# Performance work log

Measured on AMD Instinct MI355X. Metric: run time of the kernel, lower is better.

## Reference

```python
import jax, jax.numpy as jnp
import numpy as np

T = 32
TAU = 2.0
ALPHA = 2.0
V_TH = 1.0
V_RESET = 0.0
PHI = 0.05
MAX_ACTION = 1.0
STATE_DIM, ACTION_DIM = 376, 17
H1, H2 = 400, 300
BATCH = 8192


@jax.custom_vjp
def spike_fn(x):
    # Heaviside with ATan surrogate gradient (spikingjelly surrogate.ATan)
    return (x >= 0.0).astype(x.dtype)

def _spike_fwd(x):
    return spike_fn(x), x

def _spike_bwd(x, g):
    return (g * (ALPHA / 2.0) / (1.0 + (jnp.pi / 2.0 * ALPHA * x) ** 2),)

spike_fn.defvjp(_spike_fwd, _spike_bwd)


def setup_inputs() -> dict:
    key = jax.random.key(0)
    ks = jax.random.split(key, 8)
    d_in = STATE_DIM + ACTION_DIM
    s = lambda k, shape, fan: jax.random.uniform(k, shape, jnp.float32, -1.0, 1.0) / np.sqrt(fan)
    return {
        "state": jax.random.normal(ks[0], (BATCH, STATE_DIM), jnp.float32),
        "action": jax.random.normal(ks[1], (BATCH, ACTION_DIM), jnp.float32),
        "W1": s(ks[2], (d_in, H1), d_in), "b1": s(ks[3], (H1,), d_in),
        "W2": s(ks[4], (H1, H2), H1),   "b2": s(ks[5], (H2,), H1),
        "W3": s(ks[6], (H2, ACTION_DIM), H2), "b3": s(ks[7], (ACTION_DIM,), H2),
    }


def reference(state, action, W1, b1, W2, b2, W3, b3):
    # input repeated over T -> layer-1 pre-activation current is step-invariant
    inp = jnp.concatenate([state, action], axis=1)          # [B, state+action]
    x1 = inp @ W1 + b1                                      # [B, H1]
    B = state.shape[0]

    def step(carry, _):
        v1, v2, v3 = carry
        # LIF layer 1: charge v += (x - (v - v_reset))/tau, fire, hard reset
        v1 = v1 + (x1 - (v1 - V_RESET)) / TAU
        s1 = spike_fn(v1 - V_TH)
        v1 = s1 * V_RESET + (1.0 - s1) * v1
        # LIF layer 2
        x2 = s1 @ W2 + b2
        v2 = v2 + (x2 - (v2 - V_RESET)) / TAU
        s2 = spike_fn(v2 - V_TH)
        v2 = s2 * V_RESET + (1.0 - s2) * v2
        # non-spiking LIF layer 3: charge only, output membrane potential
        x3 = s2 @ W3 + b3
        v3 = v3 + (x3 - (v3 - V_RESET)) / TAU
        return (v1, v2, v3), v3

    init = (jnp.full((B, H1), V_RESET, x1.dtype),
            jnp.full((B, H2), V_RESET, x1.dtype),
            jnp.full((B, ACTION_DIM), V_RESET, x1.dtype))
    _, v3_seq = jax.lax.scan(step, init, None, length=T)    # [T, B, action_dim]
    a = v3_seq.max(axis=0)
    a = PHI * MAX_ACTION * jnp.tanh(a)
    return jnp.clip(a + action, -MAX_ACTION, MAX_ACTION)
```

## Files before the change

kernel.cpp:

```cpp
#include <hip/hip_runtime.h>
#include <math.h>

#define SDIM 376
#define ADIM 17
#define DIN  393
#define H1   400
#define H2   300
#define TSTEPS 32
#define KP 416

typedef __bf16 bf16x8 __attribute__((ext_vector_type(8)));
typedef float  f32x4  __attribute__((ext_vector_type(4)));

__global__ __launch_bounds__(256) void prep_fused(
    const float* __restrict__ state, const float* __restrict__ action,
    const float* __restrict__ W1,
    __bf16* __restrict__ inpb, __bf16* __restrict__ W1T,
    int B, int npack) {
    const int bid = blockIdx.x, tid = threadIdx.x;
    if (bid < npack) {
        int idx = bid * 256 + tid;
        int r = idx / 52, c = idx - r * 52;
        if (r >= B) return;
        int g0 = c * 8;
        float v[8];
        if (g0 + 7 < SDIM) {
            float4 a = *(const float4*)&state[r * SDIM + g0];
            float4 b = *(const float4*)&state[r * SDIM + g0 + 4];
            v[0]=a.x; v[1]=a.y; v[2]=a.z; v[3]=a.w; v[4]=b.x; v[5]=b.y; v[6]=b.z; v[7]=b.w;
        } else {
            #pragma unroll
            for (int e = 0; e < 8; ++e) {
                int k = g0 + e;
                v[e] = (k < SDIM) ? state[r * SDIM + k]
                     : (k < DIN)  ? action[r * ADIM + k - SDIM] : 0.f;
            }
        }
        bf16x8 o;
        #pragma unroll
        for (int e = 0; e < 8; ++e) o[e] = (__bf16)v[e];
        *(bf16x8*)&inpb[r * KP + g0] = o;
    } else {
        int idx = (bid - npack) * 256 + tid;
        if (idx >= H1 * KP) return;
        int n = idx / KP, k = idx - n * KP;
        W1T[idx] = (__bf16)((k < DIN) ? W1[k * H1 + n] : 0.f);
    }
}

__global__ __launch_bounds__(256) void gemm_mask(
    const __bf16* __restrict__ inpb, const __bf16* __restrict__ W1T,
    const float* __restrict__ b1, unsigned short* __restrict__ maskbuf) {
    const int tid = threadIdx.x, wave = tid >> 6, lane = tid & 63;
    const int quad = lane >> 4, l16 = lane & 15;
    const int bm0 = blockIdx.x * 64 + wave * 16;
    const int bn0 = blockIdx.y * 80;

    f32x4 acc[5];
    #pragma unroll
    for (int n = 0; n < 5; ++n) acc[n] = (f32x4){0.f, 0.f, 0.f, 0.f};

    const __bf16* ap = inpb + (size_t)(bm0 + l16) * KP + quad * 8;
    const __bf16* bp = W1T + (size_t)(bn0 + l16) * KP + quad * 8;

    #pragma unroll
    for (int k0 = 0; k0 < KP; k0 += 32) {
        bf16x8 af = *(const bf16x8*)(ap + k0);
        #pragma unroll
        for (int n = 0; n < 5; ++n) {
            bf16x8 bfrag = *(const bf16x8*)(bp + n * 16 * KP + k0);
            acc[n] = __builtin_amdgcn_mfma_f32_16x16x32_bf16(af, bfrag, acc[n], 0, 0, 0);
        }
    }

    float b1v[5];
    #pragma unroll
    for (int n = 0; n < 5; ++n) b1v[n] = b1[bn0 + n * 16 + l16];
    const int cbase = bn0 >> 4;
    #pragma unroll
    for (int n = 0; n < 5; ++n)
        #pragma unroll
        for (int reg = 0; reg < 4; ++reg) {
            unsigned long long bal = __ballot(acc[n][reg] + b1v[n] >= 0.99f);
            if (l16 == 0)
                maskbuf[(size_t)(bm0 + quad * 4 + reg) * 32 + cbase + n] =
                    (unsigned short)(bal >> (quad * 16));
        }
}

__global__ __launch_bounds__(256) void snn_actor(
    const unsigned long long* __restrict__ mask64,
    const float* __restrict__ state, const float* __restrict__ action,
    const float* __restrict__ W1, const float* __restrict__ b1,
    const float* __restrict__ W2, const float* __restrict__ b2,
    const float* __restrict__ W3, const float* __restrict__ b3,
    float* __restrict__ out) {
    const int lane = threadIdx.x & 63;
    const int row  = blockIdx.x * 4 + (threadIdx.x >> 6);

    unsigned long long mw = 0;
    if (lane < 7) {
        mw = mask64[row * 8 + lane];
        if (lane == 6) mw &= 0xFFFFULL;
    }

    const float act = (lane < ADIM) ? action[row * ADIM + lane] : 0.f;
    const float b3v = (lane < ADIM) ? b3[lane] : 0.f;

    float gv;
    {
        float v3 = 0.f, vm = -3.0e38f;
        #pragma unroll
        for (int t = 0; t < TSTEPS; ++t) { v3 += (b3v - v3) * 0.5f; vm = fmaxf(vm, v3); }
        gv = 0.05f * tanhf(vm);
    }

    float bound[5];
    #pragma unroll
    for (int c = 0; c < 5; ++c) { int j = lane + 64 * c; bound[c] = (j < H2) ? b2[j] : 0.f; }
    #pragma unroll 1
    for (int w = 0; w < 7; ++w) {
        unsigned long long m = __shfl(mw, w);
        while (m) {
            int b = __builtin_ctzll(m); m &= m - 1;
            const float* wr = W2 + (w * 64 + b) * H2;
            #pragma unroll
            for (int c = 0; c < 5; ++c) {
                int j = lane + 64 * c;
                if (j < H2) bound[c] += fmaxf(wr[j], 0.f);
            }
        }
    }
    bool ok = true;
    #pragma unroll
    for (int c = 0; c < 5; ++c) ok = ok && (bound[c] < 0.999f);
    if (__all(ok)) {
        if (lane < ADIM) out[row * ADIM + lane] = fminf(fmaxf(gv + act, -1.f), 1.f);
        return;
    }

    float x1v[7];
    #pragma unroll
    for (int s = 0; s < 7; ++s) { int col = lane + 64 * s; x1v[s] = (col < H1) ? b1[col] : 0.f; }
    for (int k = 0; k < DIN; ++k) {
        float ik = (k < SDIM) ? state[row * SDIM + k] : action[row * ADIM + k - SDIM];
        #pragma unroll
        for (int s = 0; s < 7; ++s) {
            int col = lane + 64 * s;
            if (col < H1) x1v[s] += ik * W1[k * H1 + col];
        }
    }
    float b2v[5];
    #pragma unroll
    for (int c = 0; c < 5; ++c) { int j = lane + 64 * c; b2v[c] = (j < H2) ? b2[j] : 0.f; }
    float v1[7], v2[5], v3 = 0.f, vmax = -3.0e38f;
    #pragma unroll
    for (int s = 0; s < 7; ++s) v1[s] = 0.f;
    #pragma unroll
    for (int c = 0; c < 5; ++c) v2[c] = 0.f;
    for (int t = 0; t < TSTEPS; ++t) {
        float x2[5];
        #pragma unroll
        for (int c = 0; c < 5; ++c) x2[c] = b2v[c];
        #pragma unroll
        for (int s = 0; s < 7; ++s) {
            float v = v1[s] + (x1v[s] - v1[s]) * 0.5f;
            bool sp = v >= 1.0f;
            v1[s] = sp ? 0.f : v;
            unsigned long long m = __ballot(sp);
            while (m) {
                int j = __builtin_ctzll(m); m &= m - 1;
                const float* wr = W2 + (s * 64 + j) * H2;
                #pragma unroll
                for (int c = 0; c < 5; ++c) {
                    int col = lane + 64 * c;
                    if (col < H2) x2[c] += wr[col];
                }
            }
        }
        float x3 = b3v;
        #pragma unroll
        for (int c = 0; c < 5; ++c) {
            float v = v2[c] + (x2[c] - v2[c]) * 0.5f;
            int col = lane + 64 * c;
            bool sp = (col < H2) && (v >= 1.0f);
            v2[c] = sp ? 0.f : v;
            unsigned long long m = __ballot(sp);
            while (m) {
                int j = __builtin_ctzll(m); m &= m - 1;
                if (lane < ADIM) x3 += W3[(c * 64 + j) * ADIM + lane];
            }
        }
        v3 += (x3 - v3) * 0.5f;
        vmax = fmaxf(vmax, v3);
    }
    if (lane < ADIM)
        out[row * ADIM + lane] = fminf(fmaxf(0.05f * tanhf(vmax) + act, -1.f), 1.f);
}

extern "C" void kernel_launch(void* const* d_in, const int* in_sizes, int n_in,
                              void* d_out, int out_size, void* d_ws, size_t ws_size,
                              hipStream_t stream) {
    const float* state  = (const float*)d_in[0];
    const float* action = (const float*)d_in[1];
    const float* W1     = (const float*)d_in[2];
    const float* b1     = (const float*)d_in[3];
    const float* W2     = (const float*)d_in[4];
    const float* b2     = (const float*)d_in[5];
    const float* W3     = (const float*)d_in[6];
    const float* b3     = (const float*)d_in[7];
    float* out = (float*)d_out;

    const int B = in_sizes[0] / SDIM;

    char* p = (char*)d_ws;
    __bf16* inpb = (__bf16*)p;                 p += (size_t)B * KP * 2;
    __bf16* W1T  = (__bf16*)p;                 p += (size_t)H1 * KP * 2;
    unsigned short* maskbuf = (unsigned short*)p;
    unsigned long long* mask64 = (unsigned long long*)p;

    const int npack = (B * 52 + 255) / 256;
    const int nw1t  = (H1 * KP + 255) / 256;
    prep_fused<<<npack + nw1t, 256, 0, stream>>>(state, action, W1, inpb, W1T, B, npack);
    gemm_mask<<<dim3(B / 64, 5), 256, 0, stream>>>(inpb, W1T, b1, maskbuf);
    snn_actor<<<B / 4, 256, 0, stream>>>(mask64, state, action,
                                         W1, b1, W2, b2, W3, b3, out);
}
```

Before: 109.5 us.

## Fuse bf16 packing and W1 transpose into the mask GEMM kernel

Drops the separate prep kernel that converted state/action and W1 to padded bf16 buffers in workspace. The GEMM kernel now reads fp32 state/action directly, converting to bf16 in registers, and each block stages its 80-column slice of W1 into LDS in MFMA fragment order. This removes a kernel launch and the round trip of the intermediate buffers through global memory. In exchange, every block re-reads and converts the full W1 slice (B/64 times redundantly), and the first loop iteration reads from LDS slots written by a different thread.

```diff
diff --git a/kernel.cpp b/kernel.cpp
--- a/kernel.cpp
+++ b/kernel.cpp
@@ -7,83 +7,79 @@
 #define H1   400
 #define H2   300
 #define TSTEPS 32
-#define KP 416
+#define NKT 13
 
 typedef __bf16 bf16x8 __attribute__((ext_vector_type(8)));
 typedef float  f32x4  __attribute__((ext_vector_type(4)));
 
-__global__ __launch_bounds__(256) void prep_fused(
+__global__ __launch_bounds__(256) void gemm_mask_fused(
     const float* __restrict__ state, const float* __restrict__ action,
-    const float* __restrict__ W1,
-    __bf16* __restrict__ inpb, __bf16* __restrict__ W1T,
-    int B, int npack) {
-    const int bid = blockIdx.x, tid = threadIdx.x;
-    if (bid < npack) {
-        int idx = bid * 256 + tid;
-        int r = idx / 52, c = idx - r * 52;
-        if (r >= B) return;
-        int g0 = c * 8;
-        float v[8];
-        if (g0 + 7 < SDIM) {
-            float4 a = *(const float4*)&state[r * SDIM + g0];
-            float4 b = *(const float4*)&state[r * SDIM + g0 + 4];
-            v[0]=a.x; v[1]=a.y; v[2]=a.z; v[3]=a.w; v[4]=b.x; v[5]=b.y; v[6]=b.z; v[7]=b.w;
+    const float* __restrict__ W1, const float* __restrict__ b1,
+    unsigned short* __restrict__ maskbuf) {
+    __shared__ __bf16 Bf[5 * NKT * 64 * 8];
+
+    const int tid = threadIdx.x, wave = tid >> 6, lane = tid & 63;
+    const int quad = lane >> 4, l16 = lane & 15;
+    const int bm0 = blockIdx.x * 64;
+    const int bn0 = blockIdx.y * 80;
+
+    {
+        int k = tid / 80, c = tid - (tid / 80) * 80;
+        #pragma unroll 1
+        for (int i = tid; i < 416 * 80; i += 256) {
+            float v = (k < DIN) ? W1[k * H1 + bn0 + c] : 0.f;
+            int ntile = c >> 4, kt = k >> 5, q = (k >> 3) & 3, e = k & 7;
+            Bf[(((ntile * NKT + kt) * 64) + (q << 4) + (c & 15)) * 8 + e] = (__bf16)v;
+            c += 16; k += 3;
+            if (c >= 80) { c -= 80; k += 1; }
+        }
+    }
+    __syncthreads();
+
+    const int arow = bm0 + wave * 16 + l16;
+    const float* __restrict__ srow = state + (size_t)arow * SDIM;
+    const float* __restrict__ arow_p = action + (size_t)arow * ADIM;
+
+    f32x4 acc[5];
+    #pragma unroll
+    for (int n = 0; n < 5; ++n) acc[n] = (f32x4){0.f, 0.f, 0.f, 0.f};
+
+    #pragma unroll
+    for (int kt = 0; kt < NKT; ++kt) {
+        bf16x8 af;
+        const int k0 = kt * 32 + quad * 8;
+        if (kt <= 10) {
+            float4 x = *(const float4*)(srow + k0);
+            float4 y = *(const float4*)(srow + k0 + 4);
+            af[0]=(__bf16)x.x; af[1]=(__bf16)x.y; af[2]=(__bf16)x.z; af[3]=(__bf16)x.w;
+            af[4]=(__bf16)y.x; af[5]=(__bf16)y.y; af[6]=(__bf16)y.z; af[7]=(__bf16)y.w;
         } else {
             #pragma unroll
             for (int e = 0; e < 8; ++e) {
-                int k = g0 + e;
-                v[e] = (k < SDIM) ? state[r * SDIM + k]
-                     : (k < DIN)  ? action[r * ADIM + k - SDIM] : 0.f;
-            }
-        }
-        bf16x8 o;
-        #pragma unroll
-        for (int e = 0; e < 8; ++e) o[e] = (__bf16)v[e];
-        *(bf16x8*)&inpb[r * KP + g0] = o;
-    } else {
-        int idx = (bid - npack) * 256 + tid;
-        if (idx >= H1 * KP) return;
-        int n = idx / KP, k = idx - n * KP;
-        W1T[idx] = (__bf16)((k < DIN) ? W1[k * H1 + n] : 0.f);
-    }
-}
-
-__global__ __launch_bounds__(256) void gemm_mask(
-    const __bf16* __restrict__ inpb, const __bf16* __restrict__ W1T,
-    const float* __restrict__ b1, unsigned short* __restrict__ maskbuf) {
-    const int tid = threadIdx.x, wave = tid >> 6, lane = tid & 63;
-    const int quad = lane >> 4, l16 = lane & 15;
-    const int bm0 = blockIdx.x * 64 + wave * 16;
-    const int bn0 = blockIdx.y * 80;
-
-    f32x4 acc[5];
-    #pragma unroll
-    for (int n = 0; n < 5; ++n) acc[n] = (f32x4){0.f, 0.f, 0.f, 0.f};
-
-    const __bf16* ap = inpb + (size_t)(bm0 + l16) * KP + quad * 8;
-    const __bf16* bp = W1T + (size_t)(bn0 + l16) * KP + quad * 8;
-
-    #pragma unroll
-    for (int k0 = 0; k0 < KP; k0 += 32) {
-        bf16x8 af = *(const bf16x8*)(ap + k0);
+                int k = k0 + e;
+                float v = (k < SDIM) ? srow[k] : (k < DIN) ? arow_p[k - SDIM] : 0.f;
+                af[e] = (__bf16)v;
+            }
+        }
         #pragma unroll
         for (int n = 0; n < 5; ++n) {
-            bf16x8 bfrag = *(const bf16x8*)(bp + n * 16 * KP + k0);
-            acc[n] = __builtin_amdgcn_mfma_f32_16x16x32_bf16(af, bfrag, acc[n], 0, 0, 0);
+            bf16x8 bfr = *(const bf16x8*)&Bf[(((n * NKT + kt) * 64) + lane) * 8];
+            acc[n] = __builtin_amdgcn_mfma_f32_16x16x32_bf16(af, bfr, acc[n], 0, 0, 0);
         }
     }
 
     float b1v[5];
     #pragma unroll
     for (int n = 0; n < 5; ++n) b1v[n] = b1[bn0 + n * 16 + l16];
-    const int cbase = bn0 >> 4;
+    const int cbase = blockIdx.y * 5;
+    const int mbase = bm0 + wave * 16;
     #pragma unroll
     for (int n = 0; n < 5; ++n)
         #pragma unroll
         for (int reg = 0; reg < 4; ++reg) {
             unsigned long long bal = __ballot(acc[n][reg] + b1v[n] >= 0.99f);
             if (l16 == 0)
-                maskbuf[(size_t)(bm0 + quad * 4 + reg) * 32 + cbase + n] =
+                maskbuf[(size_t)(mbase + quad * 4 + reg) * 32 + cbase + n] =
                     (unsigned short)(bal >> (quad * 16));
         }
 }
@@ -213,16 +209,10 @@
 
     const int B = in_sizes[0] / SDIM;
 
-    char* p = (char*)d_ws;
-    __bf16* inpb = (__bf16*)p;                 p += (size_t)B * KP * 2;
-    __bf16* W1T  = (__bf16*)p;                 p += (size_t)H1 * KP * 2;
-    unsigned short* maskbuf = (unsigned short*)p;
-    unsigned long long* mask64 = (unsigned long long*)p;
-
-    const int npack = (B * 52 + 255) / 256;
-    const int nw1t  = (H1 * KP + 255) / 256;
-    prep_fused<<<npack + nw1t, 256, 0, stream>>>(state, action, W1, inpb, W1T, B, npack);
-    gemm_mask<<<dim3(B / 64, 5), 256, 0, stream>>>(inpb, W1T, b1, maskbuf);
+    unsigned short* maskbuf = (unsigned short*)d_ws;
+    unsigned long long* mask64 = (unsigned long long*)d_ws;
+
+    gemm_mask_fused<<<dim3(B / 64, 5), 256, 0, stream>>>(state, action, W1, b1, maskbuf);
     snn_actor<<<B / 4, 256, 0, stream>>>(mask64, state, action,
                                          W1, b1, W2, b2, W3, b3, out);
 }
```

Measured after the change: 179.1 us. +63.5%, slower.
